# Kernel tuning notes

Measured on AMD Instinct MI355X. Metric: run time of the kernel, lower is better.

The kernel has to match this reference:

```python
import jax, jax.numpy as jnp
import numpy as np

N_NODES = 100000
N_EDGES = 1600000
IN_CH = 128
HID = 64
N_LAYERS = 4
OUT_CH = 10
NUM_GRAPHS = 128
BN_EPS = 1e-5


def setup_inputs() -> dict:
    key = jax.random.key(0)
    ks = jax.random.split(key, 24)
    s = 0.05
    inp = {
        "x": jax.random.normal(ks[0], (N_NODES, IN_CH), dtype=jnp.float32),
        "edge_index": jax.random.randint(ks[1], (2, N_EDGES), 0, N_NODES, dtype=jnp.int32),
        "batch": jnp.sort(jax.random.randint(ks[2], (N_NODES,), 0, NUM_GRAPHS, dtype=jnp.int32)),
        # GIN layer 0: MLP([IN_CH, HID, HID])
        "W1f": jax.random.normal(ks[3], (IN_CH, HID), dtype=jnp.float32) * s,
        "b1f": jnp.zeros((HID,), jnp.float32),
        "W2f": jax.random.normal(ks[4], (HID, HID), dtype=jnp.float32) * s,
        "b2f": jnp.zeros((HID,), jnp.float32),
        # GIN layers 1..3: MLP([HID, HID, HID]) each, stacked
        "W1r": jax.random.normal(ks[5], (N_LAYERS - 1, HID, HID), dtype=jnp.float32) * s,
        "b1r": jnp.zeros((N_LAYERS - 1, HID), jnp.float32),
        "W2r": jax.random.normal(ks[6], (N_LAYERS - 1, HID, HID), dtype=jnp.float32) * s,
        "b2r": jnp.zeros((N_LAYERS - 1, HID), jnp.float32),
        # JumpingKnowledge 'cat' projection: Linear(N_LAYERS*HID -> HID)
        "Wjk": jax.random.normal(ks[7], (N_LAYERS * HID, HID), dtype=jnp.float32) * s,
        "bjk": jnp.zeros((HID,), jnp.float32),
        # classifier MLP([HID, HID, OUT_CH]) with batch_norm
        "Wc1": jax.random.normal(ks[8], (HID, HID), dtype=jnp.float32) * s,
        "bc1": jnp.zeros((HID,), jnp.float32),
        "gamma": jnp.ones((HID,), jnp.float32),
        "beta": jnp.zeros((HID,), jnp.float32),
        "Wc2": jax.random.normal(ks[9], (HID, OUT_CH), dtype=jnp.float32) * s,
        "bc2": jnp.zeros((OUT_CH,), jnp.float32),
    }
    return inp


def _gin_conv(h, src, dst, W1, b1, W2, b2):
    # sum-aggregate messages from src to dst (eps = 0, so (1+eps)*x = x)
    agg = jax.ops.segment_sum(h[src], dst, num_segments=N_NODES)
    z = h + agg
    # GINConv nn: Linear -> ReLU -> Linear
    return jax.nn.relu(z @ W1 + b1) @ W2 + b2


def reference(x, edge_index, batch, W1f, b1f, W2f, b2f, W1r, b1r, W2r, b2r,
              Wjk, bjk, Wc1, bc1, gamma, beta, Wc2, bc2):
    src, dst = edge_index[0], edge_index[1]
    xs = []
    h = jax.nn.relu(_gin_conv(x, src, dst, W1f, b1f, W2f, b2f))  # post-conv act (dropout eval no-op)
    xs.append(h)
    for l in range(N_LAYERS - 1):
        h = jax.nn.relu(_gin_conv(h, src, dst, W1r[l], b1r[l], W2r[l], b2r[l]))
        xs.append(h)
    # JumpingKnowledge 'cat' + Linear
    h = jnp.concatenate(xs, axis=-1) @ Wjk + bjk            # [N, HID]
    # global add pool per graph
    pooled = jax.ops.segment_sum(h, batch, num_segments=NUM_GRAPHS)  # [G, HID]
    # classifier: Linear -> BatchNorm (batch stats) -> ReLU -> Linear
    z = pooled @ Wc1 + bc1
    mu = jnp.mean(z, axis=0)
    var = jnp.var(z, axis=0)
    z = gamma * (z - mu) * jax.lax.rsqrt(var + BN_EPS) + beta
    z = jax.nn.relu(z)
    return z @ Wc2 + bc2                                    # [G, OUT_CH]
```

## Files before the change

### kernel.cpp

```cpp
#include <hip/hip_runtime.h>
#include <hip/hip_bf16.h>

#define N_NODES    100000
#define N_EDGES    1600000
#define IN_CH      128
#define HID        64
#define N_LAYERS   4
#define OUT_CH     10
#define NUM_GRAPHS 128
#define BN_EPS     1e-5f
#define CAP        64
#define NREP       8
#define NBKT       256
#define NBUCK      196
#define EPB        2048
#define PNB        782
#define SUBCAP     2688
#define ZB         360
#define P0B        6250

typedef __hip_bfloat16 bf16;
typedef unsigned int uint32;
typedef float f32x2 __attribute__((ext_vector_type(2)));
typedef float f32x4 __attribute__((ext_vector_type(4)));

__device__ __forceinline__ float bf2f(bf16 v) { return __bfloat162float(v); }
__device__ __forceinline__ f32x2 unpk2(uint32 p) {
    f32x2 r;
    r.x = __uint_as_float(p << 16);
    r.y = __uint_as_float(p & 0xffff0000u);
    return r;
}

__global__ void zero_i(int* __restrict__ p, int n) {
    int i = blockIdx.x * 256 + threadIdx.x;
    int st = gridDim.x * 256;
    for (; i < n; i += st) p[i] = 0;
}

__global__ void stage1(const int* __restrict__ dst, int* __restrict__ ghist,
                       int* __restrict__ zp, int zn,
                       const float* __restrict__ x, const float* __restrict__ W1,
                       bf16* __restrict__ ybf) {
    const int bid = blockIdx.x;
    const int t = threadIdx.x;
    if (bid < PNB) {
        __shared__ int h[NBKT];
        h[t] = 0;
        __syncthreads();
        long base = (long)bid * EPB;
        for (int u = 0; u < 8; u++) {
            long e = base + u * 256 + t;
            if (e < N_EDGES) atomicAdd(&h[dst[e] >> 9], 1);
        }
        __syncthreads();
        if (h[t]) atomicAdd(&ghist[t], h[t]);
    } else if (bid < PNB + ZB) {
        int i = (bid - PNB) * 256 + t;
        const int st = ZB * 256;
        for (; i < zn; i += st) zp[i] = 0;
    } else {
        __shared__ __align__(16) float xshT[4][IN_CH][4];
        const int wave = t >> 6, lane = t & 63;
        const int nb = (bid - PNB - ZB) * 16 + wave * 4;
        #pragma unroll
        for (int r = 0; r < 4; r++) {
            float2 v = ((const float2*)(x + (long)(nb + r) * IN_CH))[lane];
            xshT[wave][2 * lane][r]     = v.x;
            xshT[wave][2 * lane + 1][r] = v.y;
        }
        f32x2 aA = {0.f, 0.f}, aB = {0.f, 0.f};
        #pragma unroll 8
        for (int k = 0; k < IN_CH; k++) {
            f32x4 q = *(const f32x4*)&xshT[wave][k][0];
            float w = W1[k * 64 + lane];
            f32x2 wv = {w, w};
            aA += (f32x2){q.x, q.y} * wv;
            aB += (f32x2){q.z, q.w} * wv;
        }
        ybf[(long)(nb + 0) * 64 + lane] = __float2bfloat16(aA.x);
        ybf[(long)(nb + 1) * 64 + lane] = __float2bfloat16(aA.y);
        ybf[(long)(nb + 2) * 64 + lane] = __float2bfloat16(aB.x);
        ybf[(long)(nb + 3) * 64 + lane] = __float2bfloat16(aB.y);
    }
}

__global__ void bscan(const int* __restrict__ ghist, int* __restrict__ gcursor,
                      int* __restrict__ gbase,
                      const int* __restrict__ batch, int* __restrict__ cntg,
                      bf16* __restrict__ ybfA, bf16* __restrict__ ybfB) {
    __shared__ int sh[NBKT];
    int t = threadIdx.x;
    int v = ghist[t];
    sh[t] = v;
    __syncthreads();
    for (int off = 1; off < NBKT; off <<= 1) {
        int a = (t >= off) ? sh[t - off] : 0;
        __syncthreads();
        sh[t] += a;
        __syncthreads();
    }
    gcursor[t] = sh[t] - v;
    gbase[t]   = sh[t] - v;
    if (t < NUM_GRAPHS) {
        int g = t, lo = 0, hi = N_NODES;
        while (lo < hi) { int m = (lo + hi) >> 1; if (batch[m] < g) lo = m + 1; else hi = m; }
        int lb = lo;
        lo = 0; hi = N_NODES;
        while (lo < hi) { int m = (lo + hi) >> 1; if (batch[m] < g + 1) lo = m + 1; else hi = m; }
        cntg[g] = lo - lb;
    }
    if (t < HID) {
        ybfA[(long)N_NODES * HID + t] = __float2bfloat16(0.f);
        ybfB[(long)N_NODES * HID + t] = __float2bfloat16(0.f);
    }
}

__global__ void bpart(const int* __restrict__ src, const int* __restrict__ dst,
                      int* __restrict__ gcursor, int* __restrict__ epart) {
    __shared__ int h[NBKT];
    __shared__ int cur[NBKT];
    int t = threadIdx.x;
    h[t] = 0;
    __syncthreads();
    long base = (long)blockIdx.x * EPB;
    int myd[8], mys[8];
    for (int u = 0; u < 8; u++) {
        long e = base + u * 256 + t;
        if (e < N_EDGES) {
            myd[u] = dst[e];
            mys[u] = src[e];
            atomicAdd(&h[myd[u] >> 9], 1);
        } else myd[u] = -1;
    }
    __syncthreads();
    if (h[t]) cur[t] = atomicAdd(&gcursor[t], h[t]);
    __syncthreads();
    for (int u = 0; u < 8; u++) {
        if (myd[u] >= 0) {
            int pos = atomicAdd(&cur[myd[u] >> 9], 1);
            epart[pos] = mys[u] | ((myd[u] & 511) << 17);
        }
    }
}

__global__ __launch_bounds__(256)
void bfill(const int* __restrict__ epart, const int* __restrict__ gbase,
           const int* __restrict__ ghist, int* __restrict__ cnt,
           int* __restrict__ col) {
    __shared__ int lcnt[128];
    __shared__ int loff[128];
    __shared__ int lsrc[SUBCAP];
    const int b = blockIdx.x >> 2;
    const int q = blockIdx.x & 3;
    const int t = threadIdx.x;
    const int n0 = (b << 9) + (q << 7);
    if (n0 >= N_NODES) return;
    const int nN = min(128, N_NODES - n0);
    const int base = gbase[b];
    const int m = ghist[b];
    const int lo = q << 7;

    if (t < 128) lcnt[t] = 0;
    __syncthreads();
    for (int e = t; e < m; e += 256) {
        int ln = (int)((uint32)epart[base + e] >> 17) - lo;
        if ((uint32)ln < 128u) atomicAdd(&lcnt[ln], 1);
    }
    __syncthreads();
    if (t < 128) loff[t] = lcnt[t];
    __syncthreads();
    for (int off = 1; off < 128; off <<= 1) {
        int a = (t < 128 && t >= off) ? loff[t - off] : 0;
        __syncthreads();
        if (t < 128) loff[t] += a;
        __syncthreads();
    }
    int ex = 0;
    if (t < 128) ex = loff[t] - lcnt[t];
    __syncthreads();
    if (t < 128) { loff[t] = ex; lcnt[t] = 0; }
    __syncthreads();
    for (int e = t; e < m; e += 256) {
        uint32 v = (uint32)epart[base + e];
        int ln = (int)(v >> 17) - lo;
        if ((uint32)ln < 128u) {
            int slot = atomicAdd(&lcnt[ln], 1);
            lsrc[loff[ln] + slot] = (int)(v & 0x1FFFFu);
        }
    }
    __syncthreads();
    if (t < nN) {
        int deg = lcnt[t];
        int st  = loff[t];
        int n   = n0 + t;
        cnt[n] = deg;
        int d32 = (deg + 31) & ~31;
        int* row = col + n * CAP;
        for (int s4 = 0; s4 < d32; s4 += 4) {
            int4 qv;
            qv.x = (s4 + 0 < deg) ? lsrc[st + s4 + 0] : N_NODES;
            qv.y = (s4 + 1 < deg) ? lsrc[st + s4 + 1] : N_NODES;
            qv.z = (s4 + 2 < deg) ? lsrc[st + s4 + 2] : N_NODES;
            qv.w = (s4 + 3 < deg) ? lsrc[st + s4 + 3] : N_NODES;
            *(int4*)(row + s4) = qv;
        }
    }
}

template <bool HAS_NEXT>
__global__ __launch_bounds__(256, 6)
void layer_fused(const bf16* __restrict__ ybf, const int* __restrict__ cnt,
                 const int* __restrict__ col, const int* __restrict__ batch,
                 const float* __restrict__ b1, const float* __restrict__ W2,
                 const float* __restrict__ b2, const float* __restrict__ W1n,
                 bf16* __restrict__ ynext, float* __restrict__ pooled_l) {
    __shared__ float csh[4][8][65];
    __shared__ float tsh[4][4][HID];
    __shared__ float hsh[4][4][HID];
    __shared__ float psh[4][HID];
    const int wave = threadIdx.x >> 6, lane = threadIdx.x & 63;
    const int eg = lane >> 3;
    const int j  = lane & 7;
    const uint32 joff = (uint32)j * 16u;
    const int nA = blockIdx.x * 16;
    const int nW = nA + wave * 4;
    const char* ybase = (const char*)ybf;

    #pragma unroll
    for (int r = 0; r < 4; r++) {
        const int n = __builtin_amdgcn_readfirstlane(nW + r);
        const int deg32 = __builtin_amdgcn_readfirstlane((cnt[n] + 31) & ~31);
        const int s = n * CAP;
        float acc[8] = {0.f, 0.f, 0.f, 0.f, 0.f, 0.f, 0.f, 0.f};
        for (int i = 0; i < deg32; i += 32) {
            uint4 p[4];
            #pragma unroll
            for (int t = 0; t < 4; t++) {
                int c = col[s + i + 8 * t + eg];
                uint32 off = ((uint32)c << 7) + joff;
                p[t] = *(const uint4*)(ybase + off);
            }
            #pragma unroll
            for (int t = 0; t < 4; t++) {
                f32x2 f0 = unpk2(p[t].x); acc[0] += f0.x; acc[1] += f0.y;
                f32x2 f1 = unpk2(p[t].y); acc[2] += f1.x; acc[3] += f1.y;
                f32x2 f2 = unpk2(p[t].z); acc[4] += f2.x; acc[5] += f2.y;
                f32x2 f3 = unpk2(p[t].w); acc[6] += f3.x; acc[7] += f3.y;
            }
        }
        #pragma unroll
        for (int d = 0; d < 8; d++) csh[wave][eg][8 * j + d] = acc[d];
        float sumv = 0.f;
        #pragma unroll
        for (int ee = 0; ee < 8; ee++) sumv += csh[wave][ee][lane];
        float t = bf2f(ybf[(long)n * 64 + lane]) + b1[lane] + sumv;
        tsh[wave][r][lane] = fmaxf(t, 0.f);
    }

    float hv0, hv1, hv2, hv3;
    {
        const float bb = b2[lane];
        float h0 = bb, h1 = bb, h2 = bb, h3 = bb;
        for (int k = 0; k < 64; k += 4) {
            float4 t0 = *(const float4*)&tsh[wave][0][k];
            float4 t1 = *(const float4*)&tsh[wave][1][k];
            float4 t2 = *(const float4*)&tsh[wave][2][k];
            float4 t3 = *(const float4*)&tsh[wave][3][k];
            float w0 = W2[(k + 0) * 64 + lane];
            float w1 = W2[(k + 1) * 64 + lane];
            float w2 = W2[(k + 2) * 64 + lane];
            float w3 = W2[(k + 3) * 64 + lane];
            h0 += t0.x * w0 + t0.y * w1 + t0.z * w2 + t0.w * w3;
            h1 += t1.x * w0 + t1.y * w1 + t1.z * w2 + t1.w * w3;
            h2 += t2.x * w0 + t2.y * w1 + t2.z * w2 + t2.w * w3;
            h3 += t3.x * w0 + t3.y * w1 + t3.z * w2 + t3.w * w3;
        }
        hv0 = fmaxf(h0, 0.f); hv1 = fmaxf(h1, 0.f);
        hv2 = fmaxf(h2, 0.f); hv3 = fmaxf(h3, 0.f);
    }
    hsh[wave][0][lane] = hv0;
    hsh[wave][1][lane] = hv1;
    hsh[wave][2][lane] = hv2;
    hsh[wave][3][lane] = hv3;

    if (HAS_NEXT) {
        float y0 = 0.f, y1 = 0.f, y2 = 0.f, y3 = 0.f;
        for (int k = 0; k < 64; k += 4) {
            float4 g0 = *(const float4*)&hsh[wave][0][k];
            float4 g1 = *(const float4*)&hsh[wave][1][k];
            float4 g2 = *(const float4*)&hsh[wave][2][k];
            float4 g3 = *(const float4*)&hsh[wave][3][k];
            float w0 = W1n[(k + 0) * 64 + lane];
            float w1 = W1n[(k + 1) * 64 + lane];
            float w2 = W1n[(k + 2) * 64 + lane];
            float w3 = W1n[(k + 3) * 64 + lane];
            y0 += g0.x * w0 + g0.y * w1 + g0.z * w2 + g0.w * w3;
            y1 += g1.x * w0 + g1.y * w1 + g1.z * w2 + g1.w * w3;
            y2 += g2.x * w0 + g2.y * w1 + g2.z * w2 + g2.w * w3;
            y3 += g3.x * w0 + g3.y * w1 + g3.z * w2 + g3.w * w3;
        }
        ynext[(long)(nW + 0) * 64 + lane] = __float2bfloat16(y0);
        ynext[(long)(nW + 1) * 64 + lane] = __float2bfloat16(y1);
        ynext[(long)(nW + 2) * 64 + lane] = __float2bfloat16(y2);
        ynext[(long)(nW + 3) * 64 + lane] = __float2bfloat16(y3);
    }

    const int gA = __builtin_amdgcn_readfirstlane(batch[nA]);
    const int gZ = __builtin_amdgcn_readfirstlane(batch[nA + 15]);
    float* rep = pooled_l + (long)(blockIdx.x & (NREP - 1)) * NUM_GRAPHS * HID;
    if (gA == gZ) {
        psh[wave][lane] = (hv0 + hv1) + (hv2 + hv3);
        __syncthreads();
        if (wave == 0) {
            float ssum = (psh[0][lane] + psh[1][lane]) + (psh[2][lane] + psh[3][lane]);
            atomicAdd(&rep[gA * 64 + lane], ssum);
        }
    } else {
        const int g0 = __builtin_amdgcn_readfirstlane(batch[nW + 0]);
        atomicAdd(&rep[g0 * 64 + lane], hv0);
        const int g1 = __builtin_amdgcn_readfirstlane(batch[nW + 1]);
        atomicAdd(&rep[g1 * 64 + lane], hv1);
        const int g2 = __builtin_amdgcn_readfirstlane(batch[nW + 2]);
        atomicAdd(&rep[g2 * 64 + lane], hv2);
        const int g3 = __builtin_amdgcn_readfirstlane(batch[nW + 3]);
        atomicAdd(&rep[g3 * 64 + lane], hv3);
    }
}

__global__ void jk_cls1(const float* __restrict__ pooled, const int* __restrict__ cntg,
                        const float* __restrict__ Wjk, const float* __restrict__ bjk,
                        const float* __restrict__ Wc1, const float* __restrict__ bc1,
                        float* __restrict__ Z, float* __restrict__ zstats) {
    __shared__ __align__(16) float sh[4][HID];
    __shared__ float pacc[4][HID];
    __shared__ __align__(16) float pj[HID];
    __shared__ float zacc[4][HID];
    const int g = blockIdx.x;
    const int wave = threadIdx.x >> 6, j = threadIdx.x & 63;

    float s = 0.f;
    for (int r = 0; r < NREP; r++)
        s += pooled[((long)(wave * NREP + r) * NUM_GRAPHS + g) * 64 + j];
    sh[wave][j] = s;
    const float* W = Wjk + (long)wave * HID * 64;
    float a = 0.f;
    for (int k = 0; k < 64; k += 4) {
        f32x4 sv = *(const f32x4*)&sh[wave][k];
        a += sv.x * W[(k + 0) * 64 + j];
        a += sv.y * W[(k + 1) * 64 + j];
        a += sv.z * W[(k + 2) * 64 + j];
        a += sv.w * W[(k + 3) * 64 + j];
    }
    pacc[wave][j] = a;
    __syncthreads();

    if (wave == 0)
        pj[j] = (float)cntg[g] * bjk[j]
              + (pacc[0][j] + pacc[1][j]) + (pacc[2][j] + pacc[3][j]);
    __syncthreads();

    float z = 0.f;
    for (int k = 16 * wave; k < 16 * wave + 16; k += 4) {
        f32x4 pv = *(const f32x4*)&pj[k];
        z += pv.x * Wc1[(k + 0) * 64 + j];
        z += pv.y * Wc1[(k + 1) * 64 + j];
        z += pv.z * Wc1[(k + 2) * 64 + j];
        z += pv.w * Wc1[(k + 3) * 64 + j];
    }
    zacc[wave][j] = z;
    __syncthreads();
    if (wave == 0) {
        float zv = bc1[j] + (zacc[0][j] + zacc[1][j]) + (zacc[2][j] + zacc[3][j]);
        Z[g * 64 + j] = zv;
        atomicAdd(&zstats[j], zv);
        atomicAdd(&zstats[HID + j], zv * zv);
    }
}

__global__ void cls2(const float* __restrict__ Z, const float* __restrict__ zstats,
                     const float* __restrict__ gamma, const float* __restrict__ beta,
                     const float* __restrict__ Wc2, const float* __restrict__ bc2,
                     float* __restrict__ out) {
    __shared__ float v[HID];
    const int g = blockIdx.x, j = threadIdx.x;
    float mu = zstats[j] * (1.f / NUM_GRAPHS);
    float var = zstats[HID + j] * (1.f / NUM_GRAPHS) - mu * mu;
    float rs = rsqrtf(var + BN_EPS);
    float zv = Z[g * 64 + j];
    v[j] = fmaxf(gamma[j] * (zv - mu) * rs + beta[j], 0.f);
    if (j < OUT_CH) {
        float acc = bc2[j];
        for (int k = 0; k < 64; k++) acc += v[k] * Wc2[k * OUT_CH + j];
        out[g * OUT_CH + j] = acc;
    }
}

extern "C" void kernel_launch(void* const* d_in, const int* in_sizes, int n_in,
                              void* d_out, int out_size, void* d_ws, size_t ws_size,
                              hipStream_t stream) {
    const float* x     = (const float*)d_in[0];
    const int*   ei    = (const int*)d_in[1];
    const int*   batch = (const int*)d_in[2];
    const float* W1f   = (const float*)d_in[3];
    const float* b1f   = (const float*)d_in[4];
    const float* W2f   = (const float*)d_in[5];
    const float* b2f   = (const float*)d_in[6];
    const float* W1r   = (const float*)d_in[7];
    const float* b1r   = (const float*)d_in[8];
    const float* W2r   = (const float*)d_in[9];
    const float* b2r   = (const float*)d_in[10];
    const float* Wjk   = (const float*)d_in[11];
    const float* bjk   = (const float*)d_in[12];
    const float* Wc1   = (const float*)d_in[13];
    const float* bc1   = (const float*)d_in[14];
    const float* gamma = (const float*)d_in[15];
    const float* beta  = (const float*)d_in[16];
    const float* Wc2   = (const float*)d_in[17];
    const float* bc2   = (const float*)d_in[18];

    const int* src = ei;
    const int* dst = ei + N_EDGES;

    float* ws        = (float*)d_ws;
    float* Z         = ws;
    bf16*  ybfA      = (bf16*)(Z + NUM_GRAPHS * HID);
    bf16*  ybfB      = ybfA + (long)(N_NODES + 1) * HID;
    int*   cnt       = (int*)(ybfB + (long)(N_NODES + 1) * HID);
    float* pooled    = (float*)(cnt + N_NODES);
    int*   gcursor   = (int*)(pooled + (long)N_LAYERS * NREP * NUM_GRAPHS * HID);
    int*   gbase     = gcursor + NBKT;
    int*   cntg      = gbase + NBKT;
    float* zstats    = (float*)(cntg + NUM_GRAPHS);
    int*   ghist     = (int*)(zstats + 2 * HID);
    int*   col       = ghist + NBKT;
    int*   epart     = col + (long)N_NODES * CAP;
    const int ZN = N_LAYERS * NREP * NUM_GRAPHS * HID
                 + 2 * NBKT + NUM_GRAPHS + 2 * HID;

    zero_i<<<1, 256, 0, stream>>>(ghist, NBKT);

    stage1<<<PNB + ZB + P0B, 256, 0, stream>>>(dst, ghist, (int*)pooled, ZN,
                                               x, W1f, ybfA);
    bscan<<<1, 256, 0, stream>>>(ghist, gcursor, gbase, batch, cntg, ybfA, ybfB);
    bpart<<<PNB, 256, 0, stream>>>(src, dst, gcursor, epart);
    bfill<<<NBUCK * 4, 256, 0, stream>>>(epart, gbase, ghist, cnt, col);

    const int NB = N_NODES / 16;
    const long PL = (long)NREP * NUM_GRAPHS * HID;
    layer_fused<true><<<NB, 256, 0, stream>>>(
        ybfA, cnt, col, batch, b1f, W2f, b2f,
        W1r, ybfB, pooled);
    layer_fused<true><<<NB, 256, 0, stream>>>(
        ybfB, cnt, col, batch, b1r, W2r, b2r,
        W1r + (long)1 * HID * HID, ybfA, pooled + 1 * PL);
    layer_fused<true><<<NB, 256, 0, stream>>>(
        ybfA, cnt, col, batch, b1r + HID, W2r + (long)1 * HID * HID, b2r + HID,
        W1r + (long)2 * HID * HID, ybfB, pooled + 2 * PL);
    layer_fused<false><<<NB, 256, 0, stream>>>(
        ybfB, cnt, col, batch, b1r + 2 * HID, W2r + (long)2 * HID * HID, b2r + 2 * HID,
        nullptr, nullptr, pooled + 3 * PL);

    jk_cls1<<<NUM_GRAPHS, 256, 0, stream>>>(pooled, cntg, Wjk, bjk, Wc1, bc1,
                                            Z, zstats);
    cls2<<<NUM_GRAPHS, 64, 0, stream>>>(Z, zstats, gamma, beta, Wc2, bc2,
                                        (float*)d_out);
}
```

Before: 422.7 us.

## Use bf16 MFMA for per-layer dense matmuls with pre-packed weight fragments

Replaces the scalar FP32 W2 and next-layer W1 matmuls in the fused GIN layer kernel with 16x16x32 bf16 MFMA instructions. The weights are pre-converted to bf16 and packed into the MFMA fragment layout by extra blocks in stage1. Intermediate activations are staged in shared memory as bf16 with block-wide syncs. The pooling reduction now uses cross-lane shuffles. This cuts the ALU and weight-load cost of the dense part, at the cost of lower precision for the hidden activations and weights and added __syncthreads between waves.

```diff
diff --git a/kernel.cpp b/kernel.cpp
--- a/kernel.cpp
+++ b/kernel.cpp
@@ -18,11 +18,13 @@
 #define SUBCAP     2688
 #define ZB         360
 #define P0B        6250
+#define NWMAT      7
 
 typedef __hip_bfloat16 bf16;
 typedef unsigned int uint32;
 typedef float f32x2 __attribute__((ext_vector_type(2)));
 typedef float f32x4 __attribute__((ext_vector_type(4)));
+typedef short s16x8 __attribute__((ext_vector_type(8)));
 
 __device__ __forceinline__ float bf2f(bf16 v) { return __bfloat162float(v); }
 __device__ __forceinline__ f32x2 unpk2(uint32 p) {
@@ -31,6 +33,10 @@
     r.y = __uint_as_float(p & 0xffff0000u);
     return r;
 }
+__device__ __forceinline__ short f2bs(float f) {
+    bf16 b = __float2bfloat16(f);
+    return *reinterpret_cast<short*>(&b);
+}
 
 __global__ void zero_i(int* __restrict__ p, int n) {
     int i = blockIdx.x * 256 + threadIdx.x;
@@ -41,7 +47,9 @@
 __global__ void stage1(const int* __restrict__ dst, int* __restrict__ ghist,
                        int* __restrict__ zp, int zn,
                        const float* __restrict__ x, const float* __restrict__ W1,
-                       bf16* __restrict__ ybf) {
+                       bf16* __restrict__ ybf,
+                       const float* __restrict__ W2f, const float* __restrict__ W2r,
+                       const float* __restrict__ W1r, bf16* __restrict__ wfrag) {
     const int bid = blockIdx.x;
     const int t = threadIdx.x;
     if (bid < PNB) {
@@ -59,7 +67,7 @@
         int i = (bid - PNB) * 256 + t;
         const int st = ZB * 256;
         for (; i < zn; i += st) zp[i] = 0;
-    } else {
+    } else if (bid < PNB + ZB + P0B) {
         __shared__ __align__(16) float xshT[4][IN_CH][4];
         const int wave = t >> 6, lane = t & 63;
         const int nb = (bid - PNB - ZB) * 16 + wave * 4;
@@ -82,6 +90,21 @@
         ybf[(long)(nb + 1) * 64 + lane] = __float2bfloat16(aA.y);
         ybf[(long)(nb + 2) * 64 + lane] = __float2bfloat16(aB.x);
         ybf[(long)(nb + 3) * 64 + lane] = __float2bfloat16(aB.y);
+    } else {
+        int mi = bid - (PNB + ZB + P0B);
+        const float* W = (mi == 0) ? W2f
+                       : (mi <= 3) ? W2r + (long)(mi - 1) * HID * HID
+                                   : W1r + (long)(mi - 4) * HID * HID;
+        bf16* out = wfrag + mi * HID * HID;
+        for (int u = 0; u < 2; u++) {
+            int idx = u * 256 + t;
+            int lane = idx & 63, tk = idx >> 6;
+            int kbase = (tk & 1) * 32 + 8 * (lane >> 4);
+            int c = (tk >> 1) * 16 + (lane & 15);
+            #pragma unroll
+            for (int j = 0; j < 8; j++)
+                out[idx * 8 + j] = __float2bfloat16(W[(kbase + j) * 64 + c]);
+        }
     }
 }
 
@@ -212,13 +235,12 @@
 __global__ __launch_bounds__(256, 6)
 void layer_fused(const bf16* __restrict__ ybf, const int* __restrict__ cnt,
                  const int* __restrict__ col, const int* __restrict__ batch,
-                 const float* __restrict__ b1, const float* __restrict__ W2,
-                 const float* __restrict__ b2, const float* __restrict__ W1n,
+                 const float* __restrict__ b1, const bf16* __restrict__ w2frag,
+                 const float* __restrict__ b2, const bf16* __restrict__ w1nfrag,
                  bf16* __restrict__ ynext, float* __restrict__ pooled_l) {
     __shared__ float csh[4][8][65];
-    __shared__ float tsh[4][4][HID];
-    __shared__ float hsh[4][4][HID];
-    __shared__ float psh[4][HID];
+    __shared__ __align__(16) short Tsh[16][72];
+    __shared__ __align__(16) short Hsh[16][72];
     const int wave = threadIdx.x >> 6, lane = threadIdx.x & 63;
     const int eg = lane >> 3;
     const int j  = lane & 7;
@@ -254,77 +276,54 @@
         float sumv = 0.f;
         #pragma unroll
         for (int ee = 0; ee < 8; ee++) sumv += csh[wave][ee][lane];
-        float t = bf2f(ybf[(long)n * 64 + lane]) + b1[lane] + sumv;
-        tsh[wave][r][lane] = fmaxf(t, 0.f);
-    }
-
-    float hv0, hv1, hv2, hv3;
-    {
-        const float bb = b2[lane];
-        float h0 = bb, h1 = bb, h2 = bb, h3 = bb;
-        for (int k = 0; k < 64; k += 4) {
-            float4 t0 = *(const float4*)&tsh[wave][0][k];
-            float4 t1 = *(const float4*)&tsh[wave][1][k];
-            float4 t2 = *(const float4*)&tsh[wave][2][k];
-            float4 t3 = *(const float4*)&tsh[wave][3][k];
-            float w0 = W2[(k + 0) * 64 + lane];
-            float w1 = W2[(k + 1) * 64 + lane];
-            float w2 = W2[(k + 2) * 64 + lane];
-            float w3 = W2[(k + 3) * 64 + lane];
-            h0 += t0.x * w0 + t0.y * w1 + t0.z * w2 + t0.w * w3;
-            h1 += t1.x * w0 + t1.y * w1 + t1.z * w2 + t1.w * w3;
-            h2 += t2.x * w0 + t2.y * w1 + t2.z * w2 + t2.w * w3;
-            h3 += t3.x * w0 + t3.y * w1 + t3.z * w2 + t3.w * w3;
-        }
-        hv0 = fmaxf(h0, 0.f); hv1 = fmaxf(h1, 0.f);
-        hv2 = fmaxf(h2, 0.f); hv3 = fmaxf(h3, 0.f);
-    }
-    hsh[wave][0][lane] = hv0;
-    hsh[wave][1][lane] = hv1;
-    hsh[wave][2][lane] = hv2;
-    hsh[wave][3][lane] = hv3;
+        float tv = bf2f(ybf[(long)n * 64 + lane]) + b1[lane] + sumv;
+        Tsh[4 * wave + r][lane] = f2bs(fmaxf(tv, 0.f));
+    }
+    __syncthreads();
+
+    const int c15 = lane & 15, g16 = lane >> 4;
+    s16x8 a0 = *(const s16x8*)((const char*)Tsh + c15 * 144 + g16 * 16);
+    s16x8 a1 = *(const s16x8*)((const char*)Tsh + c15 * 144 + g16 * 16 + 64);
+    const s16x8* w2q = (const s16x8*)w2frag;
+    f32x4 hacc = {0.f, 0.f, 0.f, 0.f};
+    hacc = __builtin_amdgcn_mfma_f32_16x16x32_bf16(a0, w2q[(wave * 2 + 0) * 64 + lane], hacc, 0, 0, 0);
+    hacc = __builtin_amdgcn_mfma_f32_16x16x32_bf16(a1, w2q[(wave * 2 + 1) * 64 + lane], hacc, 0, 0, 0);
+    const float bb = b2[16 * wave + c15];
+    float hv[4];
+    #pragma unroll
+    for (int i = 0; i < 4; i++) hv[i] = fmaxf(hacc[i] + bb, 0.f);
 
     if (HAS_NEXT) {
-        float y0 = 0.f, y1 = 0.f, y2 = 0.f, y3 = 0.f;
-        for (int k = 0; k < 64; k += 4) {
-            float4 g0 = *(const float4*)&hsh[wave][0][k];
-            float4 g1 = *(const float4*)&hsh[wave][1][k];
-            float4 g2 = *(const float4*)&hsh[wave][2][k];
-            float4 g3 = *(const float4*)&hsh[wave][3][k];
-            float w0 = W1n[(k + 0) * 64 + lane];
-            float w1 = W1n[(k + 1) * 64 + lane];
-            float w2 = W1n[(k + 2) * 64 + lane];
-            float w3 = W1n[(k + 3) * 64 + lane];
-            y0 += g0.x * w0 + g0.y * w1 + g0.z * w2 + g0.w * w3;
-            y1 += g1.x * w0 + g1.y * w1 + g1.z * w2 + g1.w * w3;
-            y2 += g2.x * w0 + g2.y * w1 + g2.z * w2 + g2.w * w3;
-            y3 += g3.x * w0 + g3.y * w1 + g3.z * w2 + g3.w * w3;
-        }
-        ynext[(long)(nW + 0) * 64 + lane] = __float2bfloat16(y0);
-        ynext[(long)(nW + 1) * 64 + lane] = __float2bfloat16(y1);
-        ynext[(long)(nW + 2) * 64 + lane] = __float2bfloat16(y2);
-        ynext[(long)(nW + 3) * 64 + lane] = __float2bfloat16(y3);
+        #pragma unroll
+        for (int i = 0; i < 4; i++)
+            Hsh[4 * g16 + i][16 * wave + c15] = f2bs(hv[i]);
+        __syncthreads();
+        s16x8 h0 = *(const s16x8*)((const char*)Hsh + c15 * 144 + g16 * 16);
+        s16x8 h1 = *(const s16x8*)((const char*)Hsh + c15 * 144 + g16 * 16 + 64);
+        const s16x8* w1q = (const s16x8*)w1nfrag;
+        f32x4 yac = {0.f, 0.f, 0.f, 0.f};
+        yac = __builtin_amdgcn_mfma_f32_16x16x32_bf16(h0, w1q[(wave * 2 + 0) * 64 + lane], yac, 0, 0, 0);
+        yac = __builtin_amdgcn_mfma_f32_16x16x32_bf16(h1, w1q[(wave * 2 + 1) * 64 + lane], yac, 0, 0, 0);
+        #pragma unroll
+        for (int i = 0; i < 4; i++)
+            ynext[(long)(nA + 4 * g16 + i) * 64 + 16 * wave + c15] = __float2bfloat16(yac[i]);
     }
 
     const int gA = __builtin_amdgcn_readfirstlane(batch[nA]);
     const int gZ = __builtin_amdgcn_readfirstlane(batch[nA + 15]);
     float* rep = pooled_l + (long)(blockIdx.x & (NREP - 1)) * NUM_GRAPHS * HID;
     if (gA == gZ) {
-        psh[wave][lane] = (hv0 + hv1) + (hv2 + hv3);
-        __syncthreads();
-        if (wave == 0) {
-            float ssum = (psh[0][lane] + psh[1][lane]) + (psh[2][lane] + psh[3][lane]);
-            atomicAdd(&rep[gA * 64 + lane], ssum);
-        }
+        float ps = (hv[0] + hv[1]) + (hv[2] + hv[3]);
+        ps += __shfl_xor(ps, 32);
+        ps += __shfl_xor(ps, 16);
+        if (g16 == 0)
+            atomicAdd(&rep[gA * 64 + 16 * wave + c15], ps);
     } else {
-        const int g0 = __builtin_amdgcn_readfirstlane(batch[nW + 0]);
-        atomicAdd(&rep[g0 * 64 + lane], hv0);
-        const int g1 = __builtin_amdgcn_readfirstlane(batch[nW + 1]);
-        atomicAdd(&rep[g1 * 64 + lane], hv1);
-        const int g2 = __builtin_amdgcn_readfirstlane(batch[nW + 2]);
-        atomicAdd(&rep[g2 * 64 + lane], hv2);
-        const int g3 = __builtin_amdgcn_readfirstlane(batch[nW + 3]);
-        atomicAdd(&rep[g3 * 64 + lane], hv3);
+        #pragma unroll
+        for (int i = 0; i < 4; i++) {
+            int gb = batch[nA + 4 * g16 + i];
+            atomicAdd(&rep[gb * 64 + 16 * wave + c15], hv[i]);
+        }
     }
 }
 
@@ -435,30 +434,32 @@
     int*   ghist     = (int*)(zstats + 2 * HID);
     int*   col       = ghist + NBKT;
     int*   epart     = col + (long)N_NODES * CAP;
+    bf16*  wfrag     = (bf16*)(epart + N_EDGES);
     const int ZN = N_LAYERS * NREP * NUM_GRAPHS * HID
                  + 2 * NBKT + NUM_GRAPHS + 2 * HID;
 
     zero_i<<<1, 256, 0, stream>>>(ghist, NBKT);
 
-    stage1<<<PNB + ZB + P0B, 256, 0, stream>>>(dst, ghist, (int*)pooled, ZN,
-                                               x, W1f, ybfA);
+    stage1<<<PNB + ZB + P0B + NWMAT, 256, 0, stream>>>(
+        dst, ghist, (int*)pooled, ZN, x, W1f, ybfA, W2f, W2r, W1r, wfrag);
     bscan<<<1, 256, 0, stream>>>(ghist, gcursor, gbase, batch, cntg, ybfA, ybfB);
     bpart<<<PNB, 256, 0, stream>>>(src, dst, gcursor, epart);
     bfill<<<NBUCK * 4, 256, 0, stream>>>(epart, gbase, ghist, cnt, col);
 
     const int NB = N_NODES / 16;
     const long PL = (long)NREP * NUM_GRAPHS * HID;
+    const int WM = HID * HID;
     layer_fused<true><<<NB, 256, 0, stream>>>(
-        ybfA, cnt, col, batch, b1f, W2f, b2f,
-        W1r, ybfB, pooled);
+        ybfA, cnt, col, batch, b1f, wfrag + 0 * WM, b2f,
+        wfrag + 4 * WM, ybfB, pooled);
     layer_fused<true><<<NB, 256, 0, stream>>>(
-        ybfB, cnt, col, batch, b1r, W2r, b2r,
-        W1r + (long)1 * HID * HID, ybfA, pooled + 1 * PL);
+        ybfB, cnt, col, batch, b1r, wfrag + 1 * WM, b2r,
+        wfrag + 5 * WM, ybfA, pooled + 1 * PL);
     layer_fused<true><<<NB, 256, 0, stream>>>(
-        ybfA, cnt, col, batch, b1r + HID, W2r + (long)1 * HID * HID, b2r + HID,
-        W1r + (long)2 * HID * HID, ybfB, pooled + 2 * PL);
+        ybfA, cnt, col, batch, b1r + HID, wfrag + 2 * WM, b2r + HID,
+        wfrag + 6 * WM, ybfB, pooled + 2 * PL);
     layer_fused<false><<<NB, 256, 0, stream>>>(
-        ybfB, cnt, col, batch, b1r + 2 * HID, W2r + (long)2 * HID * HID, b2r + 2 * HID,
+        ybfB, cnt, col, batch, b1r + 2 * HID, wfrag + 3 * WM, b2r + 2 * HID,
         nullptr, nullptr, pooled + 3 * PL);
 
     jk_cls1<<<NUM_GRAPHS, 256, 0, stream>>>(pooled, cntg, Wjk, bjk, Wc1, bc1,
```

Result: faster. 378.4 us (-10.5%).
